# Performance work log

Hardware: AMD Instinct MI355X
Metric: run time of the kernel (lower is better)

The kernel has to match this reference:

```python
import jax, jax.numpy as jnp
import numpy as np

RADIUS = 0.2
MAX_SAMPLES = 32  # max_samples_per_query


def ball_query(coords, queries, radius, k):
    """coords: [B,Np,3], queries: [B,Nq,3] -> idxs: [B,Nq,k] (first-k in index order,
    empty slots filled with the first valid index, or 0 if no neighbor -- matches
    the standard PointNet++ CUDA ball_query semantics)."""
    Np = coords.shape[1]
    # squared distances [B, Nq, Np]
    diff = queries[:, :, None, :] - coords[:, None, :, :]
    d2 = jnp.sum(diff * diff, axis=-1)
    mask = d2 < radius * radius
    # keys: point index if in-ball else sentinel Np; smallest k keys = first k valid indices
    keys = jnp.where(mask, jnp.arange(Np, dtype=jnp.int32), Np)
    neg_top, _ = jax.lax.top_k(-keys, k)           # largest of -keys == smallest keys
    sorted_keys = -neg_top                          # [B, Nq, k], ascending
    valid = sorted_keys < Np
    first = jnp.where(valid[..., 0:1], sorted_keys[..., 0:1], 0)
    return jnp.where(valid, sorted_keys, first)


def setup_inputs() -> dict:
    key = jax.random.key(0)
    k1, k2, k3, k4 = jax.random.split(key, 4)
    B, Np, Nq, C, Ct = 4, 8192, 2048, 64, 64
    return {
        "points_coords": jax.random.uniform(k1, (B, Np, 3), dtype=jnp.float32),
        "points_features": jax.random.normal(k2, (B, C, Np), dtype=jnp.float32),
        "points_t_embed": jax.random.normal(k3, (B, Ct, Np), dtype=jnp.float32),
        "queries": jax.random.uniform(k4, (B, Nq, 3), dtype=jnp.float32),
    }


def reference(points_coords, points_features, points_t_embed, queries):
    B, Np, _ = points_coords.shape
    Nq = queries.shape[1]
    K = MAX_SAMPLES
    idxs = ball_query(points_coords, queries, RADIUS, K)          # [B,Nq,K] int32
    flat = idxs.reshape(B, Nq * K)
    # grouped coords: gather along point dim then center on queries -> [B,Nq,K,3]
    grouped_coords = jnp.take_along_axis(points_coords, flat[:, :, None], axis=1)
    grouped_coords = grouped_coords.reshape(B, Nq, K, 3) - queries[:, :, None, :]
    # grouped features: gather channel-first along point dim -> [B,C,Nq,K]
    C = points_features.shape[1]
    grouped_features = jnp.take_along_axis(points_features, flat[:, None, :], axis=2)
    grouped_features = grouped_features.reshape(B, C, Nq, K)
    # use_coords=True: prepend centered coords as channels
    grouped_features = jnp.concatenate(
        [grouped_coords.transpose(0, 3, 1, 2), grouped_features], axis=1)  # [B,3+C,Nq,K]
    # t_embed gather -> [B,Ct,Nq,K]
    Ct = points_t_embed.shape[1]
    t_embed = jnp.take_along_axis(points_t_embed, flat[:, None, :], axis=2)
    t_embed = t_embed.reshape(B, Ct, Nq, K)
    return grouped_features, t_embed
```

## Files before the change

kernel.cpp:

```cpp
#include <hip/hip_runtime.h>

constexpr int kB  = 4;
constexpr int kNp = 8192;
constexpr int kNq = 2048;
constexpr int kK  = 32;
constexpr float kR2 = (float)(0.2 * 0.2);

typedef float v4f __attribute__((ext_vector_type(4)));
typedef int   v4i __attribute__((ext_vector_type(4)));

__global__ __launch_bounds__(256) void coords_soa_kernel(
    const float* __restrict__ coords, float* __restrict__ cb3)
{
    const int t = blockIdx.x * 256 + threadIdx.x;
    const int b = t >> 13;
    const int p = t & (kNp - 1);
    const float x = coords[(size_t)t * 3 + 0];
    const float y = coords[(size_t)t * 3 + 1];
    const float z = coords[(size_t)t * 3 + 2];
    float* o = cb3 + (size_t)b * 3 * kNp;
    o[0 * kNp + p] = x;
    o[1 * kNp + p] = y;
    o[2 * kNp + p] = z;
}

__global__ __launch_bounds__(256) void ball_query_kernel(
    const float* __restrict__ cb3,
    const float* __restrict__ queries,
    int* __restrict__ idxs,
    float* __restrict__ out)
{
    const int wave = (int)((blockIdx.x * blockDim.x + threadIdx.x) >> 6);
    const int lane = threadIdx.x & 63;
    const int w    = threadIdx.x >> 6;
    const int b    = wave >> 11;
    const int q    = wave & (kNq - 1);

    const float qx = queries[(b * kNq + q) * 3 + 0];
    const float qy = queries[(b * kNq + q) * 3 + 1];
    const float qz = queries[(b * kNq + q) * 3 + 2];

    const float* __restrict__ cbx = cb3 + (size_t)b * 3 * kNp;
    const float* __restrict__ cby = cbx + kNp;
    const float* __restrict__ cbz = cby + kNp;
    const v4f* __restrict__ cbx4 = (const v4f*)cbx;
    const v4f* __restrict__ cby4 = (const v4f*)cby;
    const v4f* __restrict__ cbz4 = (const v4f*)cbz;

    __shared__ int s_idx[4][kK];

    const unsigned long long lt = (1ull << lane) - 1ull;
    int cnt = 0;
    for (int base = 0; base < kNp; base += 256) {
        const int vi = (base >> 2) + lane;
        const v4f X = cbx4[vi];
        const v4f Y = cby4[vi];
        const v4f Z = cbz4[vi];

        bool in[4];
        unsigned long long m[4];
#pragma unroll
        for (int j = 0; j < 4; ++j) {
            const float dx = __fsub_rn(qx, X[j]);
            const float dy = __fsub_rn(qy, Y[j]);
            const float dz = __fsub_rn(qz, Z[j]);
            const float d2 = __fadd_rn(
                __fadd_rn(__fmul_rn(dx, dx), __fmul_rn(dy, dy)),
                __fmul_rn(dz, dz));
            in[j] = d2 < kR2;
            m[j] = __ballot(in[j]);
        }

        int pre = cnt + __popcll(m[0] & lt) + __popcll(m[1] & lt)
                      + __popcll(m[2] & lt) + __popcll(m[3] & lt);
        int local = 0;
#pragma unroll
        for (int j = 0; j < 4; ++j) {
            if (in[j]) {
                const int slot = pre + local;
                if (slot < kK) s_idx[w][slot] = base + 4 * lane + j;
                ++local;
            }
        }
        cnt += __popcll(m[0]) + __popcll(m[1])
             + __popcll(m[2]) + __popcll(m[3]);
        if (cnt >= kK) break;
    }

    if (lane < kK) {
        int v;
        if (cnt == 0)        v = 0;
        else if (lane < cnt) v = s_idx[w][lane];
        else                 v = s_idx[w][0];
        idxs[(size_t)wave * kK + lane] = v;

        const int k = lane;
        float* gf = out + ((size_t)(b * 67) * kNq + q) * kK + k;
        gf[(size_t)0 * kNq * kK] = __fsub_rn(cbx[v], qx);
        gf[(size_t)1 * kNq * kK] = __fsub_rn(cby[v], qy);
        gf[(size_t)2 * kNq * kK] = __fsub_rn(cbz[v], qz);
    }
}

__global__ __launch_bounds__(256) void gather_kernel(
    const float* __restrict__ feat,
    const float* __restrict__ temb,
    const int*   __restrict__ idxs,
    float* __restrict__ out)
{
    const int blk = blockIdx.x;
    const int b   = blk >> 7;
    const int j   = blk & 127;

    const float* src;
    float* dst;
    if (j < 64) {
        src = feat + ((size_t)b * 64 + j) * kNp;
        dst = out + (size_t)(b * 67 + 3 + j) * (kNq * kK);
    } else {
        src = temb + ((size_t)b * 64 + (j - 64)) * kNp;
        dst = out + (size_t)kB * 67 * kNq * kK
                  + (size_t)(b * 64 + (j - 64)) * (kNq * kK);
    }

    __shared__ float row[kNp];
    {
        const v4f* s4 = (const v4f*)src;
        v4f* r4 = (v4f*)row;
#pragma unroll
        for (int i = 0; i < kNp / 4 / 256; ++i)
            r4[i * 256 + threadIdx.x] = s4[i * 256 + threadIdx.x];
    }
    __syncthreads();

    const v4i* id4 = (const v4i*)(idxs + (size_t)b * kNq * kK);
    v4f* d4 = (v4f*)dst;
    constexpr int total4 = kNq * kK / 4;
#pragma unroll 4
    for (int e = threadIdx.x; e < total4; e += 256) {
        const v4i id = id4[e];
        v4f v;
        v.x = row[id.x];
        v.y = row[id.y];
        v.z = row[id.z];
        v.w = row[id.w];
        d4[e] = v;
    }
}

extern "C" void kernel_launch(void* const* d_in, const int* in_sizes, int n_in,
                              void* d_out, int out_size, void* d_ws, size_t ws_size,
                              hipStream_t stream) {
    const float* coords  = (const float*)d_in[0];
    const float* feats   = (const float*)d_in[1];
    const float* temb    = (const float*)d_in[2];
    const float* queries = (const float*)d_in[3];
    float* out = (float*)d_out;

    int*   idxs = (int*)d_ws;
    float* cb3  = (float*)((char*)d_ws + (size_t)kB * kNq * kK * 4);

    coords_soa_kernel<<<kB * kNp / 256, 256, 0, stream>>>(coords, cb3);
    ball_query_kernel<<<kB * kNq / 4, 256, 0, stream>>>(cb3, queries, idxs, out);
    gather_kernel<<<kB * 128, 256, 0, stream>>>(feats, temb, idxs, out);
}
```

Before: 177.7 us.

## Prefetch ball-query coords, split gather per channel, use nontemporal stores

The ball-query loop now loads the next 256-point coordinate chunk into registers before working on the current one, to hide global load latency. The gather kernel splits each channel row into two blocks, doubling the grid from 512 to 1024 blocks so more of the GPU is busy. Each block still stages the full 32 KB source row into LDS, so that staging work is done twice per row. Output stores and source-row loads use nontemporal hints to limit cache pollution from the large streaming output.

```diff
diff --git a/kernel.cpp b/kernel.cpp
--- a/kernel.cpp
+++ b/kernel.cpp
@@ -51,11 +51,16 @@
 
     const unsigned long long lt = (1ull << lane) - 1ull;
     int cnt = 0;
+
+    v4f X = cbx4[lane];
+    v4f Y = cby4[lane];
+    v4f Z = cbz4[lane];
+
     for (int base = 0; base < kNp; base += 256) {
-        const int vi = (base >> 2) + lane;
-        const v4f X = cbx4[vi];
-        const v4f Y = cby4[vi];
-        const v4f Z = cbz4[vi];
+        const int nvi = (base + 256 < kNp) ? (((base + 256) >> 2) + lane) : lane;
+        const v4f Xn = cbx4[nvi];
+        const v4f Yn = cby4[nvi];
+        const v4f Zn = cbz4[nvi];
 
         bool in[4];
         unsigned long long m[4];
@@ -84,6 +89,8 @@
         }
         cnt += __popcll(m[0]) + __popcll(m[1])
              + __popcll(m[2]) + __popcll(m[3]);
+
+        X = Xn; Y = Yn; Z = Zn;
         if (cnt >= kK) break;
     }
 
@@ -96,9 +103,9 @@
 
         const int k = lane;
         float* gf = out + ((size_t)(b * 67) * kNq + q) * kK + k;
-        gf[(size_t)0 * kNq * kK] = __fsub_rn(cbx[v], qx);
-        gf[(size_t)1 * kNq * kK] = __fsub_rn(cby[v], qy);
-        gf[(size_t)2 * kNq * kK] = __fsub_rn(cbz[v], qz);
+        __builtin_nontemporal_store(__fsub_rn(cbx[v], qx), gf + (size_t)0 * kNq * kK);
+        __builtin_nontemporal_store(__fsub_rn(cby[v], qy), gf + (size_t)1 * kNq * kK);
+        __builtin_nontemporal_store(__fsub_rn(cbz[v], qz), gf + (size_t)2 * kNq * kK);
     }
 }
 
@@ -109,8 +116,10 @@
     float* __restrict__ out)
 {
     const int blk = blockIdx.x;
-    const int b   = blk >> 7;
-    const int j   = blk & 127;
+    const int seg = blk & 1;
+    const int bc  = blk >> 1;
+    const int b   = bc >> 7;
+    const int j   = bc & 127;
 
     const float* src;
     float* dst;
@@ -129,22 +138,24 @@
         v4f* r4 = (v4f*)row;
 #pragma unroll
         for (int i = 0; i < kNp / 4 / 256; ++i)
-            r4[i * 256 + threadIdx.x] = s4[i * 256 + threadIdx.x];
+            r4[i * 256 + threadIdx.x] =
+                __builtin_nontemporal_load(s4 + i * 256 + threadIdx.x);
     }
     __syncthreads();
 
-    const v4i* id4 = (const v4i*)(idxs + (size_t)b * kNq * kK);
-    v4f* d4 = (v4f*)dst;
     constexpr int total4 = kNq * kK / 4;
+    constexpr int seg4   = total4 / 2;
+    const v4i* id4 = (const v4i*)(idxs + (size_t)b * kNq * kK) + seg * seg4;
+    v4f* d4 = (v4f*)dst + seg * seg4;
 #pragma unroll 4
-    for (int e = threadIdx.x; e < total4; e += 256) {
+    for (int e = threadIdx.x; e < seg4; e += 256) {
         const v4i id = id4[e];
         v4f v;
         v.x = row[id.x];
         v.y = row[id.y];
         v.z = row[id.z];
         v.w = row[id.w];
-        d4[e] = v;
+        __builtin_nontemporal_store(v, d4 + e);
     }
 }
 
@@ -162,5 +173,5 @@
 
     coords_soa_kernel<<<kB * kNp / 256, 256, 0, stream>>>(coords, cb3);
     ball_query_kernel<<<kB * kNq / 4, 256, 0, stream>>>(cb3, queries, idxs, out);
-    gather_kernel<<<kB * 128, 256, 0, stream>>>(feats, temb, idxs, out);
+    gather_kernel<<<kB * 128 * 2, 256, 0, stream>>>(feats, temb, idxs, out);
 }
```

Measured after the change: 177.4 us. No clear change (-0.2%).
